# Kernel optimization log

Hardware: AMD Instinct MI355X
Metric: run time of the kernel (lower is better)

## Reference

```python
import jax, jax.numpy as jnp
import numpy as np

SLOPE = 25.0  # snntorch surrogate.fast_sigmoid default slope
NUM_STEPS = 15

@jax.custom_vjp
def spike(x):
    # Heaviside forward, fast-sigmoid surrogate backward
    return (x > 0).astype(x.dtype)

def _spike_fwd(x):
    return spike(x), x

def _spike_bwd(x, g):
    return (g / (SLOPE * jnp.abs(x) + 1.0) ** 2,)

spike.defvjp(_spike_fwd, _spike_bwd)


def setup_inputs() -> dict:
    p, hidden, B = 97, 512, 32768
    key = jax.random.key(0)
    ks = jax.random.split(key, 6)
    s1 = 1.0 / np.sqrt(2 * hidden)
    s2 = 1.0 / np.sqrt(hidden)
    return {
        "x": jax.random.randint(ks[0], (B, 2), 0, p, dtype=jnp.int64 if jax.config.jax_enable_x64 else jnp.int32),
        "embed_w": jax.random.normal(ks[1], (p, hidden), jnp.float32),
        "W1": jax.random.uniform(ks[2], (hidden, 2 * hidden), jnp.float32, -s1, s1),
        "b1": jax.random.uniform(ks[3], (hidden,), jnp.float32, -s1, s1),
        "W2": jax.random.uniform(ks[4], (p, hidden), jnp.float32, -s2, s2),
        "b2": jax.random.uniform(ks[5], (p,), jnp.float32, -s2, s2),
        "beta1": jnp.float32(0.85),
        "beta2": jnp.float32(0.85),
        "thr1": jnp.float32(1.0),
        "thr2": jnp.float32(1.0),
    }


def reference(x, embed_w, W1, b1, W2, b2, beta1, beta2, thr1, thr2):
    # parameter clamps (done in-place under no_grad in torch)
    beta1 = jnp.clip(beta1, 0.1, 0.9)
    beta2 = jnp.clip(beta2, 0.1, 0.9)
    thr1 = jnp.maximum(thr1, 0.1)
    thr2 = jnp.maximum(thr2, 0.1)

    B = x.shape[0]
    hidden = embed_w.shape[1]
    p = W2.shape[0]

    emb = embed_w[x].reshape(B, 2 * hidden)          # [B, 2H]
    cur1 = emb @ W1.T + b1                           # constant across steps [B, H]

    def step(carry, _):
        mem1, mem2 = carry
        # lif1: Leaky, reset_mechanism='subtract'; reset computed from prev mem (detached)
        reset = jax.lax.stop_gradient((mem1 - thr1 > 0).astype(mem1.dtype))
        mem1 = jnp.clip(beta1, 0.0, 1.0) * mem1 + cur1 - reset * thr1
        spk1 = spike(mem1 - thr1)                    # [B, H]
        cur2 = spk1 @ W2.T + b2                      # [B, p]
        # lif2: reset_mechanism='none'
        mem2 = jnp.clip(beta2, 0.0, 1.0) * mem2 + cur2
        return (mem1, mem2), None

    mem1 = jnp.zeros((B, hidden), cur1.dtype)
    mem2 = jnp.zeros((B, p), cur1.dtype)
    (mem1, mem2), _ = jax.lax.scan(step, (mem1, mem2), None, length=NUM_STEPS)
    return mem2  # final membrane potential of output layer
```

## Files before the change

kernel.cpp:

```cpp
#include <hip/hip_runtime.h>
#include <cstddef>

#define PMOD 97
#define HID 512
#define NPAIR 9409
#define NSTEPS 15
#define CAP 64

typedef __attribute__((ext_vector_type(8))) short short8;
typedef __attribute__((ext_vector_type(4))) short short4_t;
typedef __attribute__((ext_vector_type(4))) float f32x4;

static __device__ __forceinline__ unsigned short f2bf_rn(float f) {
    unsigned u = __float_as_uint(f);
    u += 0x7FFFu + ((u >> 16) & 1u);
    return (unsigned short)(u >> 16);
}
static __device__ __forceinline__ float bf2f(unsigned short h) {
    return __uint_as_float(((unsigned)h) << 16);
}
static __device__ __forceinline__ void split_hilo(const float* __restrict__ p,
                                                  short8& hi, short8& lo) {
    const float4 v0 = *(const float4*)p;
    const float4 v1 = *(const float4*)(p + 4);
    const float vv[8] = {v0.x, v0.y, v0.z, v0.w, v1.x, v1.y, v1.z, v1.w};
#pragma unroll
    for (int q = 0; q < 8; ++q) {
        const unsigned short hb = f2bf_rn(vv[q]);
        hi[q] = (short)hb;
        lo[q] = (short)f2bf_rn(vv[q] - bf2f(hb));
    }
}

__global__ __launch_bounds__(256) void k_abm(const float* __restrict__ embed,
                                             const float* __restrict__ W1,
                                             const float* __restrict__ W2,
                                             const float* __restrict__ b1,
                                             short* __restrict__ w2bf,
                                             float* __restrict__ Ap,
                                             float* __restrict__ Bm) {
    __shared__ f32x4 red[3][64];

    const int t = threadIdx.x;
    const int lane = t & 63;
    const int kq = t >> 6;

    const int gid = blockIdx.x * 256 + t;
    if (gid < PMOD * HID / 4) {
        const float4 v = ((const float4*)W2)[gid];
        const float vv[4] = {v.x, v.y, v.z, v.w};
        short4_t h4;
#pragma unroll
        for (int q = 0; q < 4; ++q) h4[q] = (short)f2bf_rn(vv[q]);
        *(short4_t*)(w2bf + gid * 4) = h4;
    }

    const int mt = blockIdx.x >> 6;
    const int ng = blockIdx.x & 63;
    int e = mt * 16 + (lane & 15);
    if (e > PMOD - 1) e = PMOD - 1;
    const int n = ng * 16 + (lane & 15);
    const int h = n & 511;
    const int half = n >> 9;
    const int kbase = kq * 128 + (lane >> 4) * 8;

    f32x4 acc = (f32x4){0.f, 0.f, 0.f, 0.f};
#pragma unroll
    for (int kt = 0; kt < 4; ++kt) {
        const int k = kbase + kt * 32;
        short8 ahi, alo, bhi, blo;
        split_hilo(embed + (size_t)e * HID + k, ahi, alo);
        split_hilo(W1 + (size_t)h * 1024 + half * HID + k, bhi, blo);
        acc = __builtin_amdgcn_mfma_f32_16x16x32_bf16(ahi, bhi, acc, 0, 0, 0);
        acc = __builtin_amdgcn_mfma_f32_16x16x32_bf16(alo, bhi, acc, 0, 0, 0);
        acc = __builtin_amdgcn_mfma_f32_16x16x32_bf16(ahi, blo, acc, 0, 0, 0);
    }

    if (kq != 0) red[kq - 1][lane] = acc;
    __syncthreads();
    if (kq == 0) {
        acc += red[0][lane];
        acc += red[1][lane];
        acc += red[2][lane];
        const float bias = half ? 0.f : b1[h];
#pragma unroll
        for (int reg = 0; reg < 4; ++reg) {
            const int er = mt * 16 + (lane >> 4) * 4 + reg;
            if (er < PMOD) {
                if (half == 0) Ap[(size_t)er * HID + h] = acc[reg] + bias;
                else           Bm[(size_t)er * HID + h] = acc[reg];
            }
        }
    }
}

__global__ __launch_bounds__(1024) void k_mega(const float* __restrict__ Ap,
                                               const float* __restrict__ Bm,
                                               const short* __restrict__ w2bf,
                                               const float* __restrict__ b2,
                                               const float* __restrict__ pbeta1,
                                               const float* __restrict__ pbeta2,
                                               const float* __restrict__ pthr1,
                                               const int* __restrict__ x,
                                               int nB,
                                               float* __restrict__ out) {
    __shared__ short8 wfrag[16][64];
    __shared__ f32x4 red[3][7][64];
    __shared__ float ptile[16][112];
    __shared__ int lcnt[16];
    __shared__ int lblist[16][CAP];

    const float beta1 = fminf(fmaxf(pbeta1[0], 0.1f), 0.9f);
    const float beta2 = fminf(fmaxf(pbeta2[0], 0.1f), 0.9f);
    const float thr   = fmaxf(pthr1[0], 0.1f);

    const int t = threadIdx.x;
    const int lane = t & 63;
    const int w = t >> 6;
    const int pblk = blockIdx.x * 16;

    if (t < 16) lcnt[t] = 0;

    const int pid0 = pblk + (lane & 15);
    const int pid  = (pid0 < NPAIR) ? pid0 : (NPAIR - 1);
    const unsigned i = (unsigned)pid / PMOD;
    const unsigned j = (unsigned)pid - i * PMOD;

    {
        const int kt = w;
        const int h = kt * 32 + (lane >> 4) * 8;
        const float* ap = Ap + (size_t)i * HID + h;
        const float* bp = Bm + (size_t)j * HID + h;
        const float4 a0 = *(const float4*)ap;
        const float4 a1 = *(const float4*)(ap + 4);
        const float4 g0 = *(const float4*)bp;
        const float4 g1 = *(const float4*)(bp + 4);
        float c[8] = {a0.x + g0.x, a0.y + g0.y, a0.z + g0.z, a0.w + g0.w,
                      a1.x + g1.x, a1.y + g1.y, a1.z + g1.z, a1.w + g1.w};
        float cm[8], m[8], wv[8];
        bool sb[8];
#pragma unroll
        for (int q = 0; q < 8; ++q) {
            cm[q] = c[q] - thr; m[q] = 0.f; wv[q] = 0.f; sb[q] = false;
        }
        for (int s = 0; s < NSTEPS; ++s) {
#pragma unroll
            for (int q = 0; q < 8; ++q) {
                const float cadj = sb[q] ? cm[q] : c[q];
                m[q] = fmaf(beta1, m[q], cadj);
                sb[q] = m[q] > thr;
                wv[q] = fmaf(beta2, wv[q], sb[q] ? 1.f : 0.f);
            }
        }
        short8 af;
#pragma unroll
        for (int q = 0; q < 8; ++q) af[q] = (short)f2bf_rn(wv[q]);
        wfrag[kt][lane] = af;
    }
    __syncthreads();

    const int kq = w & 3;
    const int ns = w >> 2;
    f32x4 acc[2];
#pragma unroll
    for (int q = 0; q < 2; ++q) acc[q] = (f32x4){0.f, 0.f, 0.f, 0.f};

#pragma unroll
    for (int kk = 0; kk < 4; ++kk) {
        const int kt = kq * 4 + kk;
        const short8 af = wfrag[kt][lane];
        const int k = kt * 32 + (lane >> 4) * 8;
#pragma unroll
        for (int q = 0; q < 2; ++q) {
            const int nt = ns * 2 + q;
            if (nt < 7) {
                const int o0 = nt * 16 + (lane & 15);
                const int oc = (o0 < PMOD) ? o0 : (PMOD - 1);
                const short8 bf = *(const short8*)(w2bf + (size_t)oc * HID + k);
                acc[q] = __builtin_amdgcn_mfma_f32_16x16x32_bf16(af, bf, acc[q], 0, 0, 0);
            }
        }
    }

    if (kq != 0) {
#pragma unroll
        for (int q = 0; q < 2; ++q) {
            const int nt = ns * 2 + q;
            if (nt < 7) red[kq - 1][nt][lane] = acc[q];
        }
    }

    for (int it = 0; it < 32; ++it) {
        const int b = it * 1024 + t;
        if (b < nB) {
            const int2 xb = ((const int2*)x)[b];
            const int rel = xb.x * PMOD + xb.y - pblk;
            if ((unsigned)rel < 16u) {
                const int slot = atomicAdd(&lcnt[rel], 1);
                if (slot < CAP) lblist[rel][slot] = b;
            }
        }
    }

    __syncthreads();

    if (kq == 0) {
        float S = 0.f;
#pragma unroll
        for (int s = 0; s < NSTEPS; ++s) S = fmaf(beta2, S, 1.f);
#pragma unroll
        for (int q = 0; q < 2; ++q) {
            const int nt = ns * 2 + q;
            if (nt < 7) {
                f32x4 a = acc[q];
                a += red[0][nt][lane];
                a += red[1][nt][lane];
                a += red[2][nt][lane];
                const int o = nt * 16 + (lane & 15);
                if (o < PMOD) {
                    const float bias = b2[o] * S;
#pragma unroll
                    for (int reg = 0; reg < 4; ++reg) {
                        const int prow = (lane >> 4) * 4 + reg;
                        ptile[prow][o] = a[reg] + bias;
                    }
                }
            }
        }
    }
    __syncthreads();

    {
        const int nb = lcnt[w];
        const float v0 = ptile[w][lane];
        const float v1 = (lane < PMOD - 64) ? ptile[w][64 + lane] : 0.f;
        for (int s = 0; s < nb; ++s) {
            const int b = lblist[w][s];
            float* orow = out + (size_t)b * PMOD;
            orow[lane] = v0;
            if (lane < PMOD - 64) orow[64 + lane] = v1;
        }
    }
}

extern "C" void kernel_launch(void* const* d_in, const int* in_sizes, int n_in,
                              void* d_out, int out_size, void* d_ws, size_t ws_size,
                              hipStream_t stream) {
    const int*   x     = (const int*)d_in[0];
    const float* embed = (const float*)d_in[1];
    const float* W1    = (const float*)d_in[2];
    const float* b1    = (const float*)d_in[3];
    const float* W2    = (const float*)d_in[4];
    const float* b2    = (const float*)d_in[5];
    const float* beta1 = (const float*)d_in[6];
    const float* beta2 = (const float*)d_in[7];
    const float* thr1  = (const float*)d_in[8];

    float* out = (float*)d_out;
    const int B = in_sizes[0] / 2;

    char* ws = (char*)d_ws;
    short* w2bf = (short*)(ws);
    float* Ap   = (float*)(ws + 99584);
    float* Bm   = (float*)(ws + 298496);

    k_abm<<<448, 256, 0, stream>>>(embed, W1, W2, b1, w2bf, Ap, Bm);

    const int nblk = (NPAIR + 15) / 16;
    k_mega<<<nblk, 1024, 0, stream>>>(Ap, Bm, w2bf, b2, beta1, beta2, thr1,
                                      x, B, out);
}
```

Measured before the change: 45.80 us.

## Build global per-pair batch bucket lists once and pre-swizzle W2 fragments

Each k_mega block no longer scans all 32768 input pairs to find its own rows. Instead k_abm fills global per-pair count and list arrays once with global atomics, after a memset of the counts. W2 is repacked into MFMA fragment order so B-operand loads are contiguous. The LIF stage now gives each wave one pair across all 512 hidden units and writes an XOR-swizzled LDS tile. The main cost removed is the redundant full scan of x in about 589 blocks, paid for with an extra memset launch, global atomics and a larger workspace.

```diff
diff --git a/kernel.cpp b/kernel.cpp
--- a/kernel.cpp
+++ b/kernel.cpp
@@ -8,7 +8,6 @@
 #define CAP 64
 
 typedef __attribute__((ext_vector_type(8))) short short8;
-typedef __attribute__((ext_vector_type(4))) short short4_t;
 typedef __attribute__((ext_vector_type(4))) float f32x4;
 
 static __device__ __forceinline__ unsigned short f2bf_rn(float f) {
@@ -36,7 +35,11 @@
                                              const float* __restrict__ W1,
                                              const float* __restrict__ W2,
                                              const float* __restrict__ b1,
-                                             short* __restrict__ w2bf,
+                                             const int* __restrict__ x,
+                                             int nB,
+                                             short* __restrict__ w2f,
+                                             int* __restrict__ cnt,
+                                             int* __restrict__ blist,
                                              float* __restrict__ Ap,
                                              float* __restrict__ Bm) {
     __shared__ f32x4 red[3][64];
@@ -44,15 +47,31 @@
     const int t = threadIdx.x;
     const int lane = t & 63;
     const int kq = t >> 6;
-
     const int gid = blockIdx.x * 256 + t;
-    if (gid < PMOD * HID / 4) {
-        const float4 v = ((const float4*)W2)[gid];
-        const float vv[4] = {v.x, v.y, v.z, v.w};
-        short4_t h4;
-#pragma unroll
-        for (int q = 0; q < 4; ++q) h4[q] = (short)f2bf_rn(vv[q]);
-        *(short4_t*)(w2bf + gid * 4) = h4;
+
+    if (gid < 16 * 7 * 64) {
+        const int kt = gid / 448;
+        const int rem = gid - kt * 448;
+        const int nt = rem >> 6;
+        const int ln = rem & 63;
+        int oc = nt * 16 + (ln & 15);
+        if (oc > PMOD - 1) oc = PMOD - 1;
+        const int k = kt * 32 + (ln >> 4) * 8;
+        const float* src = W2 + (size_t)oc * HID + k;
+        const float4 v0 = *(const float4*)src;
+        const float4 v1 = *(const float4*)(src + 4);
+        const float vv[8] = {v0.x, v0.y, v0.z, v0.w, v1.x, v1.y, v1.z, v1.w};
+        short8 h8;
+#pragma unroll
+        for (int q = 0; q < 8; ++q) h8[q] = (short)f2bf_rn(vv[q]);
+        *(short8*)(w2f + (size_t)gid * 8) = h8;
+    }
+
+    if (gid < nB) {
+        const int2 xb = ((const int2*)x)[gid];
+        const int pid = xb.x * PMOD + xb.y;
+        const int slot = atomicAdd(&cnt[pid], 1);
+        if (slot < CAP) blist[pid * CAP + slot] = gid;
     }
 
     const int mt = blockIdx.x >> 6;
@@ -96,19 +115,17 @@
 
 __global__ __launch_bounds__(1024) void k_mega(const float* __restrict__ Ap,
                                                const float* __restrict__ Bm,
-                                               const short* __restrict__ w2bf,
+                                               const short* __restrict__ w2f,
                                                const float* __restrict__ b2,
                                                const float* __restrict__ pbeta1,
                                                const float* __restrict__ pbeta2,
                                                const float* __restrict__ pthr1,
-                                               const int* __restrict__ x,
-                                               int nB,
+                                               const int* __restrict__ cnt,
+                                               const int* __restrict__ blist,
                                                float* __restrict__ out) {
-    __shared__ short8 wfrag[16][64];
+    __shared__ char wkb[16 * 1024];
     __shared__ f32x4 red[3][7][64];
     __shared__ float ptile[16][112];
-    __shared__ int lcnt[16];
-    __shared__ int lblist[16][CAP];
 
     const float beta1 = fminf(fmaxf(pbeta1[0], 0.1f), 0.9f);
     const float beta2 = fminf(fmaxf(pbeta2[0], 0.1f), 0.9f);
@@ -119,18 +136,13 @@
     const int w = t >> 6;
     const int pblk = blockIdx.x * 16;
 
-    if (t < 16) lcnt[t] = 0;
-
-    const int pid0 = pblk + (lane & 15);
-    const int pid  = (pid0 < NPAIR) ? pid0 : (NPAIR - 1);
-    const unsigned i = (unsigned)pid / PMOD;
-    const unsigned j = (unsigned)pid - i * PMOD;
-
     {
-        const int kt = w;
-        const int h = kt * 32 + (lane >> 4) * 8;
-        const float* ap = Ap + (size_t)i * HID + h;
-        const float* bp = Bm + (size_t)j * HID + h;
+        int p = pblk + w;
+        if (p > NPAIR - 1) p = NPAIR - 1;
+        const unsigned i = (unsigned)p / PMOD;
+        const unsigned j = (unsigned)p - i * PMOD;
+        const float* ap = Ap + (size_t)i * HID + lane * 8;
+        const float* bp = Bm + (size_t)j * HID + lane * 8;
         const float4 a0 = *(const float4*)ap;
         const float4 a1 = *(const float4*)(ap + 4);
         const float4 g0 = *(const float4*)bp;
@@ -155,12 +167,14 @@
         short8 af;
 #pragma unroll
         for (int q = 0; q < 8; ++q) af[q] = (short)f2bf_rn(wv[q]);
-        wfrag[kt][lane] = af;
+        *(short8*)(wkb + w * 1024 + ((lane ^ (w & 7)) << 4)) = af;
     }
     __syncthreads();
 
     const int kq = w & 3;
     const int ns = w >> 2;
+    const int m16 = lane & 15;
+    const int slot = lane >> 4;
     f32x4 acc[2];
 #pragma unroll
     for (int q = 0; q < 2; ++q) acc[q] = (f32x4){0.f, 0.f, 0.f, 0.f};
@@ -168,15 +182,14 @@
 #pragma unroll
     for (int kk = 0; kk < 4; ++kk) {
         const int kt = kq * 4 + kk;
-        const short8 af = wfrag[kt][lane];
-        const int k = kt * 32 + (lane >> 4) * 8;
+        const short8 af = *(const short8*)(
+            wkb + m16 * 1024 + ((((kt << 2) + slot) ^ (m16 & 7)) << 4));
 #pragma unroll
         for (int q = 0; q < 2; ++q) {
             const int nt = ns * 2 + q;
             if (nt < 7) {
-                const int o0 = nt * 16 + (lane & 15);
-                const int oc = (o0 < PMOD) ? o0 : (PMOD - 1);
-                const short8 bf = *(const short8*)(w2bf + (size_t)oc * HID + k);
+                const short8 bf = *(const short8*)(
+                    w2f + (size_t)((kt * 7 + nt) * 64 + lane) * 8);
                 acc[q] = __builtin_amdgcn_mfma_f32_16x16x32_bf16(af, bf, acc[q], 0, 0, 0);
             }
         }
@@ -189,19 +202,6 @@
             if (nt < 7) red[kq - 1][nt][lane] = acc[q];
         }
     }
-
-    for (int it = 0; it < 32; ++it) {
-        const int b = it * 1024 + t;
-        if (b < nB) {
-            const int2 xb = ((const int2*)x)[b];
-            const int rel = xb.x * PMOD + xb.y - pblk;
-            if ((unsigned)rel < 16u) {
-                const int slot = atomicAdd(&lcnt[rel], 1);
-                if (slot < CAP) lblist[rel][slot] = b;
-            }
-        }
-    }
-
     __syncthreads();
 
     if (kq == 0) {
@@ -231,11 +231,12 @@
     __syncthreads();
 
     {
-        const int nb = lcnt[w];
+        const int p = pblk + w;
+        const int nb = (p < NPAIR) ? cnt[p] : 0;
         const float v0 = ptile[w][lane];
         const float v1 = (lane < PMOD - 64) ? ptile[w][64 + lane] : 0.f;
         for (int s = 0; s < nb; ++s) {
-            const int b = lblist[w][s];
+            const int b = blist[p * CAP + s];
             float* orow = out + (size_t)b * PMOD;
             orow[lane] = v0;
             if (lane < PMOD - 64) orow[64 + lane] = v1;
@@ -260,13 +261,17 @@
     const int B = in_sizes[0] / 2;
 
     char* ws = (char*)d_ws;
-    short* w2bf = (short*)(ws);
-    float* Ap   = (float*)(ws + 99584);
-    float* Bm   = (float*)(ws + 298496);
-
-    k_abm<<<448, 256, 0, stream>>>(embed, W1, W2, b1, w2bf, Ap, Bm);
+    int*   cnt   = (int*)(ws);
+    int*   blist = (int*)(ws + 40960);
+    short* w2f   = (short*)(ws + 2449664);
+    float* Ap    = (float*)(ws + 2564352);
+    float* Bm    = (float*)(ws + 2763008);
+
+    hipMemsetAsync(cnt, 0, NPAIR * sizeof(int), stream);
+
+    k_abm<<<448, 256, 0, stream>>>(embed, W1, W2, b1, x, B, w2f, cnt, blist, Ap, Bm);
 
     const int nblk = (NPAIR + 15) / 16;
-    k_mega<<<nblk, 1024, 0, stream>>>(Ap, Bm, w2bf, b2, beta1, beta2, thr1,
-                                      x, B, out);
-}
+    k_mega<<<nblk, 1024, 0, stream>>>(Ap, Bm, w2f, b2, beta1, beta2, thr1,
+                                      cnt, blist, out);
+}
```

New measurement: 39.74 us. 13.2% less time.
